# Kernel optimization log

Measured on AMD Instinct MI355X. Metric: run time of the kernel, lower is better.

Reference implementation:

```python
import jax, jax.numpy as jnp
import numpy as np

N_HEAD = 16
ROPE_BASE = 10000.0
RMS_EPS = 1e-6

def rms_norm(x):
    # F.rms_norm(x, (x.size(-1),)) -- no learned weight
    return x * jax.lax.rsqrt(jnp.mean(x * x, axis=-1, keepdims=True) + RMS_EPS)

def rope(x):
    # x: [B, T, H, hd]; rotate halves (non-interleaved) like the torch Rotary
    T, hd = x.shape[1], x.shape[3]
    d = hd // 2
    inv_freq = 1.0 / (ROPE_BASE ** (jnp.arange(0, hd, 2, dtype=jnp.float32) / hd))  # [d]
    t = jnp.arange(T, dtype=jnp.float32)
    freqs = jnp.outer(t, inv_freq)                       # [T, d]
    cos = jnp.cos(freqs)[None, :, None, :]
    sin = jnp.sin(freqs)[None, :, None, :]
    x1, x2 = x[..., :d], x[..., d:]
    y1 = x1 * cos + x2 * sin
    y2 = -x1 * sin + x2 * cos
    return jnp.concatenate([y1, y2], axis=-1).astype(x.dtype)

def setup_inputs() -> dict:
    key = jax.random.key(0)
    ks = jax.random.split(key, 7)
    B, T, D, H = 2, 2048, 1024, N_HEAD
    hd = D // H
    s = 0.02
    return {
        "x": jax.random.normal(ks[0], (B, T, D), jnp.float32),
        "v1": jax.random.normal(ks[1], (B, T, H, hd), jnp.float32),
        "w_q": jax.random.normal(ks[2], (D, D), jnp.float32) * s,
        "w_k": jax.random.normal(ks[3], (D, D), jnp.float32) * s,
        "w_v": jax.random.normal(ks[4], (D, D), jnp.float32) * s,
        "w_proj": jax.random.normal(ks[5], (D, D), jnp.float32) * s,
        "lamb": jnp.float32(0.5),
    }

def reference(x, v1, w_q, w_k, w_v, w_proj, lamb):
    B, T, D = x.shape
    H = N_HEAD
    hd = D // H
    q = (x @ w_q.T).reshape(B, T, H, hd)
    k = (x @ w_k.T).reshape(B, T, H, hd)
    v = (x @ w_v.T).reshape(B, T, H, hd)
    v = (1.0 - lamb) * v + lamb * v1.reshape(B, T, H, hd)
    q, k = rms_norm(q), rms_norm(k)
    q, k = rope(q), rope(k)
    scale = 1.0 / jnp.sqrt(jnp.float32(hd))
    scores = jnp.einsum('bqhd,bkhd->bhqk', q, k) * scale  # [B,H,T,T]
    causal = jnp.tril(jnp.ones((T, T), dtype=bool))
    scores = jnp.where(causal[None, None], scores, jnp.float32(-1e30))
    attn = jax.nn.softmax(scores, axis=-1)
    y = jnp.einsum('bhqk,bkhd->bqhd', attn, v).reshape(B, T, D)
    y = y @ w_proj.T
    return (y, v1)
```

## Files before the change

kernel.cpp:

```cpp
#include <hip/hip_runtime.h>

typedef __bf16 bf16x8 __attribute__((ext_vector_type(8)));
typedef float f32x4 __attribute__((ext_vector_type(4)));
typedef float f32x16 __attribute__((ext_vector_type(16)));

__device__ __forceinline__ unsigned short f2bf(float f) {
    return __builtin_bit_cast(unsigned short, (__bf16)f);
}

__device__ __forceinline__ float bf2f(unsigned short u) {
    unsigned int x = ((unsigned int)u) << 16;
    return __builtin_bit_cast(float, x);
}

__device__ __forceinline__ unsigned int packbf2(float a, float b) {
    unsigned short lo = f2bf(a), hi = f2bf(b);
    return (unsigned int)lo | ((unsigned int)hi << 16);
}

__device__ __forceinline__ bf16x8 load_frag(const unsigned short* p) {
    int4 v = *reinterpret_cast<const int4*>(p);
    return __builtin_bit_cast(bf16x8, v);
}

__device__ __forceinline__ void gload_lds16(const unsigned short* g, unsigned short* l) {
    __builtin_amdgcn_global_load_lds((const __attribute__((address_space(1))) void*)g,
                                     (__attribute__((address_space(3))) void*)l, 16, 0, 0);
}

__global__ __launch_bounds__(256) void prep_bf16(const float* __restrict__ x,
                                                 const float* __restrict__ wq,
                                                 const float* __restrict__ wk,
                                                 const float* __restrict__ wv,
                                                 const float* __restrict__ wp,
                                                 unsigned short* __restrict__ xb,
                                                 unsigned short* __restrict__ wall) {
    int i = (blockIdx.x * 256 + threadIdx.x) * 4;
    const float* src;
    unsigned short* dst;
    int soff, doff;
    if (i < (1 << 22)) {
        src = x; dst = xb; soff = i; doff = i;
    } else {
        int j = i - (1 << 22);
        int r = j >> 20;
        src = (r == 0) ? wq : ((r == 1) ? wk : ((r == 2) ? wv : wp));
        dst = wall; soff = j & 1048575; doff = j;
    }
    float4 v = *reinterpret_cast<const float4*>(&src[soff]);
    unsigned short tmp[4] = {f2bf(v.x), f2bf(v.y), f2bf(v.z), f2bf(v.w)};
    *reinterpret_cast<int2*>(&dst[doff]) = *reinterpret_cast<int2*>(tmp);
}

__global__ __launch_bounds__(256) void rope_table(float* __restrict__ cost,
                                                  float* __restrict__ sint) {
    int i = blockIdx.x * 256 + threadIdx.x;
    int t = i >> 5, d = i & 31;
    float inv = powf(10000.0f, -(float)d / 32.0f);
    float f = (float)t * inv;
    cost[i] = cosf(f);
    sint[i] = sinf(f);
}

template <bool BF16OUT>
__global__ __launch_bounds__(256) void gemm_bf16(const unsigned short* __restrict__ A,
                                                 const unsigned short* __restrict__ B,
                                                 void* __restrict__ Cv,
                                                 int N, int K) {
    __shared__ __align__(16) unsigned short As[128 * 64];
    __shared__ __align__(16) unsigned short Bs[128 * 64];
    int tid = threadIdx.x;
    int lane = tid & 63;
    int w = tid >> 6;
    int wm = w >> 1, wn = w & 1;
    int m0 = blockIdx.x * 128;
    int n0 = blockIdx.y * 128;

    f32x4 acc[4][4] = {};

    int r8 = lane >> 3;
    int csrc = (lane & 7) ^ r8;

    for (int k0 = 0; k0 < K; k0 += 64) {
        __syncthreads();
#pragma unroll
        for (int c = 0; c < 4; ++c) {
            int row = 32 * w + 8 * c + r8;
            gload_lds16(&A[(size_t)(m0 + row) * K + k0 + csrc * 8], &As[(32 * w + 8 * c) * 64]);
            gload_lds16(&B[(size_t)(n0 + row) * K + k0 + csrc * 8], &Bs[(32 * w + 8 * c) * 64]);
        }
        __syncthreads();
#pragma unroll
        for (int kk = 0; kk < 2; ++kk) {
            int col16 = kk * 4 + (lane >> 4);
            bf16x8 af[4], bfr[4];
#pragma unroll
            for (int i = 0; i < 4; ++i) {
                int row = wm * 64 + i * 16 + (lane & 15);
                af[i] = load_frag(&As[row * 64 + (col16 ^ (row & 7)) * 8]);
            }
#pragma unroll
            for (int j = 0; j < 4; ++j) {
                int row = wn * 64 + j * 16 + (lane & 15);
                bfr[j] = load_frag(&Bs[row * 64 + (col16 ^ (row & 7)) * 8]);
            }
#pragma unroll
            for (int i = 0; i < 4; ++i)
#pragma unroll
                for (int j = 0; j < 4; ++j)
                    acc[i][j] = __builtin_amdgcn_mfma_f32_16x16x32_bf16(af[i], bfr[j], acc[i][j], 0, 0, 0);
        }
    }
    int r0 = (lane >> 4) * 4;
    int cc = lane & 15;
#pragma unroll
    for (int i = 0; i < 4; ++i)
#pragma unroll
        for (int j = 0; j < 4; ++j)
#pragma unroll
            for (int r = 0; r < 4; ++r) {
                size_t m = m0 + wm * 64 + i * 16 + r0 + r;
                size_t n = n0 + wn * 64 + j * 16 + cc;
                if constexpr (BF16OUT) {
                    ((unsigned short*)Cv)[m * N + n] = f2bf(acc[i][j][r]);
                } else {
                    ((float*)Cv)[m * N + n] = acc[i][j][r];
                }
            }
}

__global__ __launch_bounds__(256) void postprocess_qk(const unsigned short* __restrict__ qkv,
                                                      const float* __restrict__ cost,
                                                      const float* __restrict__ sint,
                                                      unsigned short* __restrict__ qb,
                                                      unsigned short* __restrict__ kb) {
    int gid = blockIdx.x * 4 + (threadIdx.x >> 6);
    int lane = threadIdx.x & 63;
    int h = gid & 15;
    int t = (gid >> 4) & 2047;
    int b = gid >> 15;
    int m = b * 2048 + t;

    float q = bf2f(qkv[(size_t)m * 3072 + h * 64 + lane]);
    float k = bf2f(qkv[(size_t)m * 3072 + 1024 + h * 64 + lane]);

    float sq = q * q, sk = k * k;
    for (int msk = 1; msk < 64; msk <<= 1) {
        sq += __shfl_xor(sq, msk, 64);
        sk += __shfl_xor(sk, msk, 64);
    }
    q *= rsqrtf(sq * (1.0f / 64.0f) + 1e-6f);
    k *= rsqrtf(sk * (1.0f / 64.0f) + 1e-6f);

    int d = lane & 31;
    float c = cost[t * 32 + d], s = sint[t * 32 + d];
    float qp = __shfl_xor(q, 32, 64);
    float kp = __shfl_xor(k, 32, 64);
    float qo = (lane < 32) ? (q * c + qp * s) : (q * c - qp * s);
    float ko = (lane < 32) ? (k * c + kp * s) : (k * c - kp * s);
    qo *= 0.125f * 1.44269504088896f;

    size_t oidx = ((size_t)((b * 16 + h) * 2048 + t)) * 64 + lane;
    qb[oidx] = f2bf(qo);
    kb[oidx] = f2bf(ko);
}

__global__ __launch_bounds__(256) void lerp_transpose_v(const unsigned short* __restrict__ qkvb,
                                                        const float* __restrict__ v1,
                                                        const float* __restrict__ lamb_p,
                                                        unsigned short* __restrict__ vt,
                                                        float* __restrict__ outv1) {
    __shared__ __align__(16) unsigned short tile[64][72];
    int bh = blockIdx.y;
    int b = bh >> 4, h = bh & 15;
    int t0 = blockIdx.x * 64;
    int tid = threadIdx.x;
    int r = tid >> 3;
    int c = (tid & 7) * 8;
    float lamb = lamb_p[0];
    float oml = 1.0f - lamb;

#pragma unroll
    for (int half = 0; half < 2; ++half) {
        int row = r + half * 32;
        int m = b * 2048 + t0 + row;
        int4 vv = *reinterpret_cast<const int4*>(&qkvb[(size_t)m * 3072 + 2048 + h * 64 + c]);
        const unsigned short* vs = reinterpret_cast<const unsigned short*>(&vv);
        size_t v1i = ((size_t)m * 16 + h) * 64 + c;
        float4 va = *reinterpret_cast<const float4*>(&v1[v1i]);
        float4 vb4 = *reinterpret_cast<const float4*>(&v1[v1i + 4]);
        *reinterpret_cast<float4*>(&outv1[v1i]) = va;
        *reinterpret_cast<float4*>(&outv1[v1i + 4]) = vb4;
        float v1a[8] = {va.x, va.y, va.z, va.w, vb4.x, vb4.y, vb4.z, vb4.w};
        unsigned short tmp[8];
#pragma unroll
        for (int j = 0; j < 8; ++j) tmp[j] = f2bf(oml * bf2f(vs[j]) + lamb * v1a[j]);
        *reinterpret_cast<int4*>(&tile[row][c]) = *reinterpret_cast<int4*>(tmp);
    }
    __syncthreads();
    unsigned short* dst = vt + (size_t)bh * 64 * 2048 + t0;
    unsigned short tmp[8];
#pragma unroll
    for (int j = 0; j < 8; ++j) tmp[j] = tile[c + j][r];
    *reinterpret_cast<int4*>(&dst[(size_t)r * 2048 + c]) = *reinterpret_cast<int4*>(tmp);
#pragma unroll
    for (int j = 0; j < 8; ++j) tmp[j] = tile[c + j][r + 32];
    *reinterpret_cast<int4*>(&dst[(size_t)(r + 32) * 2048 + c]) = *reinterpret_cast<int4*>(tmp);
}

__global__ __launch_bounds__(256) void attn(const unsigned short* __restrict__ qb,
                                            const unsigned short* __restrict__ kb,
                                            const unsigned short* __restrict__ vt,
                                            unsigned short* __restrict__ pO,
                                            float* __restrict__ lsum) {
    __shared__ __align__(16) unsigned short Ks[64][72];
    __shared__ __align__(16) unsigned short Vt[64][72];
    int tid = threadIdx.x;
    int lane = tid & 63;
    int w = tid >> 6;
    int hi = lane >> 5;
    int l31 = lane & 31;

    int bid = blockIdx.x;
    int bh = bid & 31;
    int r5 = bid >> 5;
    int qt = 15 - (r5 >> 1);
    int ck = r5 & 1;
    int q0 = qt * 128;
    const size_t base = (size_t)bh * 2048 * 64;
    const unsigned short* vtb = vt + (size_t)bh * 64 * 2048;
    int ktlo = ck ? (qt + 1) : 0;
    int kthi = ck ? (2 * qt + 1) : qt;

    bf16x8 qf[4];
    int qrow = q0 + w * 32 + l31;
#pragma unroll
    for (int kd = 0; kd < 4; ++kd)
        qf[kd] = load_frag(&qb[base + (size_t)qrow * 64 + kd * 16 + hi * 8]);

    f32x16 oacc[2] = {};
    float lrun = 0.0f;

    int srow = tid >> 3;
    int scol = (tid & 7) * 8;
    int4 kr0, kr1, vr0, vr1;
#define LOADT(kt_)                                                                                    \
    do {                                                                                              \
        kr0 = *reinterpret_cast<const int4*>(&kb[base + (size_t)((kt_)*64 + srow) * 64 + scol]);      \
        kr1 = *reinterpret_cast<const int4*>(&kb[base + (size_t)((kt_)*64 + srow + 32) * 64 + scol]); \
        vr0 = *reinterpret_cast<const int4*>(&vtb[(size_t)srow * 2048 + (kt_)*64 + scol]);            \
        vr1 = *reinterpret_cast<const int4*>(&vtb[(size_t)(srow + 32) * 2048 + (kt_)*64 + scol]);     \
    } while (0)

    LOADT(ktlo);
    int qwlo = q0 + w * 32;

    for (int kt = ktlo; kt <= kthi; ++kt) {
        __syncthreads();
        *reinterpret_cast<int4*>(&Ks[srow][scol]) = kr0;
        *reinterpret_cast<int4*>(&Ks[srow + 32][scol]) = kr1;
        *reinterpret_cast<int4*>(&Vt[srow][scol]) = vr0;
        *reinterpret_cast<int4*>(&Vt[srow + 32][scol]) = vr1;
        __syncthreads();
        if (kt < kthi) LOADT(kt + 1);

        if (kt * 64 <= qwlo + 31) {
            f32x16 sacc[2] = {};
#pragma unroll
            for (int nt = 0; nt < 2; ++nt)
#pragma unroll
                for (int kd = 0; kd < 4; ++kd) {
                    bf16x8 kf = load_frag(&Ks[nt * 32 + l31][kd * 16 + hi * 8]);
                    sacc[nt] = __builtin_amdgcn_mfma_f32_32x32x16_bf16(kf, qf[kd], sacc[nt], 0, 0, 0);
                }

            bool diag = (kt * 64 + 63 > qwlo);
            float rs0 = 0.0f, rs1 = 0.0f, rs2 = 0.0f, rs3 = 0.0f;
#pragma unroll
            for (int nt = 0; nt < 2; ++nt)
#pragma unroll
                for (int r = 0; r < 16; ++r) {
                    float s = sacc[nt][r];
                    if (diag) {
                        int kvg = kt * 64 + nt * 32 + (r & 3) + 8 * (r >> 2) + 4 * hi;
                        if (kvg > qrow) s = -3.0e38f;
                    }
                    float e = __builtin_amdgcn_exp2f(s);
                    sacc[nt][r] = e;
                    if ((r & 3) == 0) rs0 += e;
                    else if ((r & 3) == 1) rs1 += e;
                    else if ((r & 3) == 2) rs2 += e;
                    else rs3 += e;
                }
            float rs = (rs0 + rs1) + (rs2 + rs3);
            rs += __shfl_xor(rs, 32, 64);
            lrun += rs;

            unsigned int wA[2][4], wB[2][4];
#pragma unroll
            for (int nt = 0; nt < 2; ++nt)
#pragma unroll
                for (int rr = 0; rr < 4; ++rr) {
                    wA[nt][rr] = packbf2(sacc[nt][4 * rr + 0], sacc[nt][4 * rr + 1]);
                    wB[nt][rr] = packbf2(sacc[nt][4 * rr + 2], sacc[nt][4 * rr + 3]);
                }

#pragma unroll
            for (int ks = 0; ks < 4; ++ks) {
                int nt = ks >> 1;
                int b2 = (ks & 1) * 2;
                auto rA = __builtin_amdgcn_permlane32_swap(wA[nt][b2], wA[nt][b2 + 1], false, false);
                auto rB = __builtin_amdgcn_permlane32_swap(wB[nt][b2], wB[nt][b2 + 1], false, false);
                uint4 pa;
                pa.x = rA[0];
                pa.y = rB[0];
                pa.z = rA[1];
                pa.w = rB[1];
                bf16x8 paf = __builtin_bit_cast(bf16x8, pa);
#pragma unroll
                for (int dt = 0; dt < 2; ++dt) {
                    bf16x8 vtf = load_frag(&Vt[dt * 32 + l31][ks * 16 + hi * 8]);
                    oacc[dt] = __builtin_amdgcn_mfma_f32_32x32x16_bf16(paf, vtf, oacc[dt], 0, 0, 0);
                }
            }
        }
    }

    unsigned short* po = pO + ((size_t)ck * 8388608u);
    float* ls = lsum + ck * 65536;
#pragma unroll
    for (int r = 0; r < 16; ++r) {
        int ql = (r & 3) + 8 * (r >> 2) + 4 * hi;
        int q = q0 + w * 32 + ql;
        size_t ro = ((size_t)bh * 2048 + q) * 64;
        po[ro + l31]      = f2bf(oacc[0][r]);
        po[ro + 32 + l31] = f2bf(oacc[1][r]);
    }
    if (hi == 0) ls[bh * 2048 + q0 + w * 32 + l31] = lrun;
#undef LOADT
}

__global__ __launch_bounds__(256) void combine(const unsigned short* __restrict__ pO,
                                               const float* __restrict__ lsum,
                                               unsigned short* __restrict__ yb) {
    int g = blockIdx.x * 256 + threadIdx.x;
    int d8 = (g & 7) * 8;
    int q  = (g >> 3) & 2047;
    int bh = g >> 14;
    int b = bh >> 4, h = bh & 15;
    size_t pi = ((size_t)bh * 2048 + q) * 64 + d8;
    int4 a = *reinterpret_cast<const int4*>(&pO[pi]);
    int4 c = *reinterpret_cast<const int4*>(&pO[8388608u + pi]);
    float l = lsum[bh * 2048 + q] + lsum[65536 + bh * 2048 + q];
    float linv = 1.0f / l;
    const unsigned short* ua = reinterpret_cast<const unsigned short*>(&a);
    const unsigned short* uc = reinterpret_cast<const unsigned short*>(&c);
    unsigned short tmp[8];
#pragma unroll
    for (int j = 0; j < 8; ++j) tmp[j] = f2bf((bf2f(ua[j]) + bf2f(uc[j])) * linv);
    *reinterpret_cast<int4*>(&yb[((size_t)(b * 2048 + q) * 16 + h) * 64 + d8]) =
        *reinterpret_cast<int4*>(tmp);
}

extern "C" void kernel_launch(void* const* d_in, const int* in_sizes, int n_in,
                              void* d_out, int out_size, void* d_ws, size_t ws_size,
                              hipStream_t stream) {
    const float* x      = (const float*)d_in[0];
    const float* v1     = (const float*)d_in[1];
    const float* w_q    = (const float*)d_in[2];
    const float* w_k    = (const float*)d_in[3];
    const float* w_v    = (const float*)d_in[4];
    const float* w_proj = (const float*)d_in[5];
    const float* lamb   = (const float*)d_in[6];
    float* out = (float*)d_out;

    char* ws = (char*)d_ws;
    unsigned short* xb      = (unsigned short*)(ws + 0);
    unsigned short* wall_b  = (unsigned short*)(ws + (8u  << 20));
    unsigned short* wqkv_b  = wall_b;
    unsigned short* wproj_b = wall_b + 3u * 1048576u;
    unsigned short* qkvb    = (unsigned short*)(ws + (16u << 20));
    unsigned short* vtp     = (unsigned short*)(ws + (40u << 20));
    unsigned short* qbuf    = (unsigned short*)(ws + (48u << 20));
    unsigned short* kbuf    = (unsigned short*)(ws + (56u << 20));
    unsigned short* ybuf    = (unsigned short*)(ws + (64u << 20));
    float*          cost    = (float*)        (ws + (72u << 20));
    float*          sint    = (float*)        (ws + (72u << 20) + 262144);
    unsigned short* pO      = (unsigned short*)(ws + 0);
    float*          lsum    = (float*)        (ws + (24u << 20));

    prep_bf16<<<8192, 256, 0, stream>>>(x, w_q, w_k, w_v, w_proj, xb, wall_b);
    rope_table<<<256, 256, 0, stream>>>(cost, sint);

    gemm_bf16<true><<<dim3(32, 24), 256, 0, stream>>>(xb, wqkv_b, (void*)qkvb, 3072, 1024);

    postprocess_qk<<<16384, 256, 0, stream>>>(qkvb, cost, sint, qbuf, kbuf);
    lerp_transpose_v<<<dim3(32, 32), 256, 0, stream>>>(qkvb, v1, lamb, vtp, out + 4194304);

    attn<<<1024, 256, 0, stream>>>(qbuf, kbuf, vtp, pO, lsum);
    combine<<<2048, 256, 0, stream>>>(pO, lsum, ybuf);

    gemm_bf16<false><<<dim3(32, 8), 256, 0, stream>>>(ybuf, wproj_b, (void*)out, 1024, 1024);
}
```

Before: 136.1 us.

## Split attention KV range into four chunks and merge small prep kernels

Attention now splits each query tile's causal key range into four balanced chunks instead of two, doubling the grid to 2048 blocks, and combine sums four partial outputs and row sums. The rope table kernel is folded into the bf16 conversion launch, and the q/k postprocess and v lerp/transpose kernels are merged into one launch. The aim is better occupancy and load balance in attention plus fewer launches. The cost is more partial-output traffic and a heavier combine step.

```diff
diff --git a/kernel.cpp b/kernel.cpp
--- a/kernel.cpp
+++ b/kernel.cpp
@@ -34,32 +34,34 @@
                                                  const float* __restrict__ wv,
                                                  const float* __restrict__ wp,
                                                  unsigned short* __restrict__ xb,
-                                                 unsigned short* __restrict__ wall) {
-    int i = (blockIdx.x * 256 + threadIdx.x) * 4;
-    const float* src;
-    unsigned short* dst;
-    int soff, doff;
-    if (i < (1 << 22)) {
-        src = x; dst = xb; soff = i; doff = i;
+                                                 unsigned short* __restrict__ wall,
+                                                 float* __restrict__ cost,
+                                                 float* __restrict__ sint) {
+    int bid = blockIdx.x;
+    if (bid < 8192) {
+        int i = (bid * 256 + threadIdx.x) * 4;
+        const float* src;
+        unsigned short* dst;
+        int soff, doff;
+        if (i < (1 << 22)) {
+            src = x; dst = xb; soff = i; doff = i;
+        } else {
+            int j = i - (1 << 22);
+            int r = j >> 20;
+            src = (r == 0) ? wq : ((r == 1) ? wk : ((r == 2) ? wv : wp));
+            dst = wall; soff = j & 1048575; doff = j;
+        }
+        float4 v = *reinterpret_cast<const float4*>(&src[soff]);
+        unsigned short tmp[4] = {f2bf(v.x), f2bf(v.y), f2bf(v.z), f2bf(v.w)};
+        *reinterpret_cast<int2*>(&dst[doff]) = *reinterpret_cast<int2*>(tmp);
     } else {
-        int j = i - (1 << 22);
-        int r = j >> 20;
-        src = (r == 0) ? wq : ((r == 1) ? wk : ((r == 2) ? wv : wp));
-        dst = wall; soff = j & 1048575; doff = j;
+        int i = (bid - 8192) * 256 + threadIdx.x;
+        int t = i >> 5, d = i & 31;
+        float inv = powf(10000.0f, -(float)d / 32.0f);
+        float f = (float)t * inv;
+        cost[i] = cosf(f);
+        sint[i] = sinf(f);
     }
-    float4 v = *reinterpret_cast<const float4*>(&src[soff]);
-    unsigned short tmp[4] = {f2bf(v.x), f2bf(v.y), f2bf(v.z), f2bf(v.w)};
-    *reinterpret_cast<int2*>(&dst[doff]) = *reinterpret_cast<int2*>(tmp);
-}
-
-__global__ __launch_bounds__(256) void rope_table(float* __restrict__ cost,
-                                                  float* __restrict__ sint) {
-    int i = blockIdx.x * 256 + threadIdx.x;
-    int t = i >> 5, d = i & 31;
-    float inv = powf(10000.0f, -(float)d / 32.0f);
-    float f = (float)t * inv;
-    cost[i] = cosf(f);
-    sint[i] = sinf(f);
 }
 
 template <bool BF16OUT>
@@ -129,83 +131,85 @@
             }
 }
 
-__global__ __launch_bounds__(256) void postprocess_qk(const unsigned short* __restrict__ qkv,
-                                                      const float* __restrict__ cost,
-                                                      const float* __restrict__ sint,
-                                                      unsigned short* __restrict__ qb,
-                                                      unsigned short* __restrict__ kb) {
-    int gid = blockIdx.x * 4 + (threadIdx.x >> 6);
-    int lane = threadIdx.x & 63;
-    int h = gid & 15;
-    int t = (gid >> 4) & 2047;
-    int b = gid >> 15;
-    int m = b * 2048 + t;
-
-    float q = bf2f(qkv[(size_t)m * 3072 + h * 64 + lane]);
-    float k = bf2f(qkv[(size_t)m * 3072 + 1024 + h * 64 + lane]);
-
-    float sq = q * q, sk = k * k;
-    for (int msk = 1; msk < 64; msk <<= 1) {
-        sq += __shfl_xor(sq, msk, 64);
-        sk += __shfl_xor(sk, msk, 64);
+__global__ __launch_bounds__(256) void post_lerp(const unsigned short* __restrict__ qkv,
+                                                 const float* __restrict__ cost,
+                                                 const float* __restrict__ sint,
+                                                 const float* __restrict__ v1,
+                                                 const float* __restrict__ lamb_p,
+                                                 unsigned short* __restrict__ qb,
+                                                 unsigned short* __restrict__ kb,
+                                                 unsigned short* __restrict__ vt,
+                                                 float* __restrict__ outv1) {
+    __shared__ __align__(16) unsigned short tile[64][72];
+    int bid = blockIdx.x;
+    if (bid < 16384) {
+        int gid = bid * 4 + (threadIdx.x >> 6);
+        int lane = threadIdx.x & 63;
+        int h = gid & 15;
+        int t = (gid >> 4) & 2047;
+        int b = gid >> 15;
+        int m = b * 2048 + t;
+
+        float q = bf2f(qkv[(size_t)m * 3072 + h * 64 + lane]);
+        float k = bf2f(qkv[(size_t)m * 3072 + 1024 + h * 64 + lane]);
+
+        float sq = q * q, sk = k * k;
+        for (int msk = 1; msk < 64; msk <<= 1) {
+            sq += __shfl_xor(sq, msk, 64);
+            sk += __shfl_xor(sk, msk, 64);
+        }
+        q *= rsqrtf(sq * (1.0f / 64.0f) + 1e-6f);
+        k *= rsqrtf(sk * (1.0f / 64.0f) + 1e-6f);
+
+        int d = lane & 31;
+        float c = cost[t * 32 + d], s = sint[t * 32 + d];
+        float qp = __shfl_xor(q, 32, 64);
+        float kp = __shfl_xor(k, 32, 64);
+        float qo = (lane < 32) ? (q * c + qp * s) : (q * c - qp * s);
+        float ko = (lane < 32) ? (k * c + kp * s) : (k * c - kp * s);
+        qo *= 0.125f * 1.44269504088896f;
+
+        size_t oidx = ((size_t)((b * 16 + h) * 2048 + t)) * 64 + lane;
+        qb[oidx] = f2bf(qo);
+        kb[oidx] = f2bf(ko);
+    } else {
+        int b2 = bid - 16384;
+        int bh = b2 >> 5;
+        int b = bh >> 4, h = bh & 15;
+        int t0 = (b2 & 31) * 64;
+        int tid = threadIdx.x;
+        int r = tid >> 3;
+        int c = (tid & 7) * 8;
+        float lamb = lamb_p[0];
+        float oml = 1.0f - lamb;
+
+#pragma unroll
+        for (int half = 0; half < 2; ++half) {
+            int row = r + half * 32;
+            int m = b * 2048 + t0 + row;
+            int4 vv = *reinterpret_cast<const int4*>(&qkv[(size_t)m * 3072 + 2048 + h * 64 + c]);
+            const unsigned short* vs = reinterpret_cast<const unsigned short*>(&vv);
+            size_t v1i = ((size_t)m * 16 + h) * 64 + c;
+            float4 va = *reinterpret_cast<const float4*>(&v1[v1i]);
+            float4 vb4 = *reinterpret_cast<const float4*>(&v1[v1i + 4]);
+            *reinterpret_cast<float4*>(&outv1[v1i]) = va;
+            *reinterpret_cast<float4*>(&outv1[v1i + 4]) = vb4;
+            float v1a[8] = {va.x, va.y, va.z, va.w, vb4.x, vb4.y, vb4.z, vb4.w};
+            unsigned short tmp[8];
+#pragma unroll
+            for (int j = 0; j < 8; ++j) tmp[j] = f2bf(oml * bf2f(vs[j]) + lamb * v1a[j]);
+            *reinterpret_cast<int4*>(&tile[row][c]) = *reinterpret_cast<int4*>(tmp);
+        }
+        __syncthreads();
+        unsigned short* dst = vt + (size_t)bh * 64 * 2048 + t0;
+        unsigned short tmp[8];
+#pragma unroll
+        for (int j = 0; j < 8; ++j) tmp[j] = tile[c + j][r];
+        *reinterpret_cast<int4*>(&dst[(size_t)r * 2048 + c]) = *reinterpret_cast<int4*>(tmp);
+#pragma unroll
+        for (int j = 0; j < 8; ++j) tmp[j] = tile[c + j][r + 32];
+        *reinterpret_cast<int4*>(&dst[(size_t)(r + 32) * 2048 + c]) = *reinterpret_cast<int4*>(tmp);
     }
-    q *= rsqrtf(sq * (1.0f / 64.0f) + 1e-6f);
-    k *= rsqrtf(sk * (1.0f / 64.0f) + 1e-6f);
-
-    int d = lane & 31;
-    float c = cost[t * 32 + d], s = sint[t * 32 + d];
-    float qp = __shfl_xor(q, 32, 64);
-    float kp = __shfl_xor(k, 32, 64);
-    float qo = (lane < 32) ? (q * c + qp * s) : (q * c - qp * s);
-    float ko = (lane < 32) ? (k * c + kp * s) : (k * c - kp * s);
-    qo *= 0.125f * 1.44269504088896f;
-
-    size_t oidx = ((size_t)((b * 16 + h) * 2048 + t)) * 64 + lane;
-    qb[oidx] = f2bf(qo);
-    kb[oidx] = f2bf(ko);
-}
-
-__global__ __launch_bounds__(256) void lerp_transpose_v(const unsigned short* __restrict__ qkvb,
-                                                        const float* __restrict__ v1,
-                                                        const float* __restrict__ lamb_p,
-                                                        unsigned short* __restrict__ vt,
-                                                        float* __restrict__ outv1) {
-    __shared__ __align__(16) unsigned short tile[64][72];
-    int bh = blockIdx.y;
-    int b = bh >> 4, h = bh & 15;
-    int t0 = blockIdx.x * 64;
-    int tid = threadIdx.x;
-    int r = tid >> 3;
-    int c = (tid & 7) * 8;
-    float lamb = lamb_p[0];
-    float oml = 1.0f - lamb;
-
-#pragma unroll
-    for (int half = 0; half < 2; ++half) {
-        int row = r + half * 32;
-        int m = b * 2048 + t0 + row;
-        int4 vv = *reinterpret_cast<const int4*>(&qkvb[(size_t)m * 3072 + 2048 + h * 64 + c]);
-        const unsigned short* vs = reinterpret_cast<const unsigned short*>(&vv);
-        size_t v1i = ((size_t)m * 16 + h) * 64 + c;
-        float4 va = *reinterpret_cast<const float4*>(&v1[v1i]);
-        float4 vb4 = *reinterpret_cast<const float4*>(&v1[v1i + 4]);
-        *reinterpret_cast<float4*>(&outv1[v1i]) = va;
-        *reinterpret_cast<float4*>(&outv1[v1i + 4]) = vb4;
-        float v1a[8] = {va.x, va.y, va.z, va.w, vb4.x, vb4.y, vb4.z, vb4.w};
-        unsigned short tmp[8];
-#pragma unroll
-        for (int j = 0; j < 8; ++j) tmp[j] = f2bf(oml * bf2f(vs[j]) + lamb * v1a[j]);
-        *reinterpret_cast<int4*>(&tile[row][c]) = *reinterpret_cast<int4*>(tmp);
-    }
-    __syncthreads();
-    unsigned short* dst = vt + (size_t)bh * 64 * 2048 + t0;
-    unsigned short tmp[8];
-#pragma unroll
-    for (int j = 0; j < 8; ++j) tmp[j] = tile[c + j][r];
-    *reinterpret_cast<int4*>(&dst[(size_t)r * 2048 + c]) = *reinterpret_cast<int4*>(tmp);
-#pragma unroll
-    for (int j = 0; j < 8; ++j) tmp[j] = tile[c + j][r + 32];
-    *reinterpret_cast<int4*>(&dst[(size_t)(r + 32) * 2048 + c]) = *reinterpret_cast<int4*>(tmp);
 }
 
 __global__ __launch_bounds__(256) void attn(const unsigned short* __restrict__ qb,
@@ -223,14 +227,15 @@
 
     int bid = blockIdx.x;
     int bh = bid & 31;
-    int r5 = bid >> 5;
-    int qt = 15 - (r5 >> 1);
-    int ck = r5 & 1;
+    int r6 = bid >> 5;
+    int qt = 15 - (r6 >> 2);
+    int ck = r6 & 3;
     int q0 = qt * 128;
     const size_t base = (size_t)bh * 2048 * 64;
     const unsigned short* vtb = vt + (size_t)bh * 64 * 2048;
-    int ktlo = ck ? (qt + 1) : 0;
-    int kthi = ck ? (2 * qt + 1) : qt;
+    int nt = 2 * qt + 2;
+    int ktlo = (ck * nt) >> 2;
+    int kthi = ((ck + 1) * nt) >> 2;
 
     bf16x8 qf[4];
     int qrow = q0 + w * 32 + l31;
@@ -252,81 +257,82 @@
         vr1 = *reinterpret_cast<const int4*>(&vtb[(size_t)(srow + 32) * 2048 + (kt_)*64 + scol]);     \
     } while (0)
 
-    LOADT(ktlo);
     int qwlo = q0 + w * 32;
-
-    for (int kt = ktlo; kt <= kthi; ++kt) {
-        __syncthreads();
-        *reinterpret_cast<int4*>(&Ks[srow][scol]) = kr0;
-        *reinterpret_cast<int4*>(&Ks[srow + 32][scol]) = kr1;
-        *reinterpret_cast<int4*>(&Vt[srow][scol]) = vr0;
-        *reinterpret_cast<int4*>(&Vt[srow + 32][scol]) = vr1;
-        __syncthreads();
-        if (kt < kthi) LOADT(kt + 1);
-
-        if (kt * 64 <= qwlo + 31) {
-            f32x16 sacc[2] = {};
-#pragma unroll
-            for (int nt = 0; nt < 2; ++nt)
-#pragma unroll
-                for (int kd = 0; kd < 4; ++kd) {
-                    bf16x8 kf = load_frag(&Ks[nt * 32 + l31][kd * 16 + hi * 8]);
-                    sacc[nt] = __builtin_amdgcn_mfma_f32_32x32x16_bf16(kf, qf[kd], sacc[nt], 0, 0, 0);
-                }
-
-            bool diag = (kt * 64 + 63 > qwlo);
-            float rs0 = 0.0f, rs1 = 0.0f, rs2 = 0.0f, rs3 = 0.0f;
-#pragma unroll
-            for (int nt = 0; nt < 2; ++nt)
-#pragma unroll
-                for (int r = 0; r < 16; ++r) {
-                    float s = sacc[nt][r];
-                    if (diag) {
-                        int kvg = kt * 64 + nt * 32 + (r & 3) + 8 * (r >> 2) + 4 * hi;
-                        if (kvg > qrow) s = -3.0e38f;
+    if (ktlo < kthi) {
+        LOADT(ktlo);
+        for (int kt = ktlo; kt < kthi; ++kt) {
+            __syncthreads();
+            *reinterpret_cast<int4*>(&Ks[srow][scol]) = kr0;
+            *reinterpret_cast<int4*>(&Ks[srow + 32][scol]) = kr1;
+            *reinterpret_cast<int4*>(&Vt[srow][scol]) = vr0;
+            *reinterpret_cast<int4*>(&Vt[srow + 32][scol]) = vr1;
+            __syncthreads();
+            if (kt + 1 < kthi) LOADT(kt + 1);
+
+            if (kt * 64 <= qwlo + 31) {
+                f32x16 sacc[2] = {};
+#pragma unroll
+                for (int ntl = 0; ntl < 2; ++ntl)
+#pragma unroll
+                    for (int kd = 0; kd < 4; ++kd) {
+                        bf16x8 kf = load_frag(&Ks[ntl * 32 + l31][kd * 16 + hi * 8]);
+                        sacc[ntl] = __builtin_amdgcn_mfma_f32_32x32x16_bf16(kf, qf[kd], sacc[ntl], 0, 0, 0);
                     }
-                    float e = __builtin_amdgcn_exp2f(s);
-                    sacc[nt][r] = e;
-                    if ((r & 3) == 0) rs0 += e;
-                    else if ((r & 3) == 1) rs1 += e;
-                    else if ((r & 3) == 2) rs2 += e;
-                    else rs3 += e;
-                }
-            float rs = (rs0 + rs1) + (rs2 + rs3);
-            rs += __shfl_xor(rs, 32, 64);
-            lrun += rs;
-
-            unsigned int wA[2][4], wB[2][4];
-#pragma unroll
-            for (int nt = 0; nt < 2; ++nt)
-#pragma unroll
-                for (int rr = 0; rr < 4; ++rr) {
-                    wA[nt][rr] = packbf2(sacc[nt][4 * rr + 0], sacc[nt][4 * rr + 1]);
-                    wB[nt][rr] = packbf2(sacc[nt][4 * rr + 2], sacc[nt][4 * rr + 3]);
-                }
-
-#pragma unroll
-            for (int ks = 0; ks < 4; ++ks) {
-                int nt = ks >> 1;
-                int b2 = (ks & 1) * 2;
-                auto rA = __builtin_amdgcn_permlane32_swap(wA[nt][b2], wA[nt][b2 + 1], false, false);
-                auto rB = __builtin_amdgcn_permlane32_swap(wB[nt][b2], wB[nt][b2 + 1], false, false);
-                uint4 pa;
-                pa.x = rA[0];
-                pa.y = rB[0];
-                pa.z = rA[1];
-                pa.w = rB[1];
-                bf16x8 paf = __builtin_bit_cast(bf16x8, pa);
-#pragma unroll
-                for (int dt = 0; dt < 2; ++dt) {
-                    bf16x8 vtf = load_frag(&Vt[dt * 32 + l31][ks * 16 + hi * 8]);
-                    oacc[dt] = __builtin_amdgcn_mfma_f32_32x32x16_bf16(paf, vtf, oacc[dt], 0, 0, 0);
+
+                bool diag = (kt * 64 + 63 > qwlo);
+                float rs0 = 0.0f, rs1 = 0.0f, rs2 = 0.0f, rs3 = 0.0f;
+#pragma unroll
+                for (int ntl = 0; ntl < 2; ++ntl)
+#pragma unroll
+                    for (int r = 0; r < 16; ++r) {
+                        float s = sacc[ntl][r];
+                        if (diag) {
+                            int kvg = kt * 64 + ntl * 32 + (r & 3) + 8 * (r >> 2) + 4 * hi;
+                            if (kvg > qrow) s = -3.0e38f;
+                        }
+                        float e = __builtin_amdgcn_exp2f(s);
+                        sacc[ntl][r] = e;
+                        if ((r & 3) == 0) rs0 += e;
+                        else if ((r & 3) == 1) rs1 += e;
+                        else if ((r & 3) == 2) rs2 += e;
+                        else rs3 += e;
+                    }
+                float rs = (rs0 + rs1) + (rs2 + rs3);
+                rs += __shfl_xor(rs, 32, 64);
+                lrun += rs;
+
+                unsigned int wA[2][4], wB[2][4];
+#pragma unroll
+                for (int ntl = 0; ntl < 2; ++ntl)
+#pragma unroll
+                    for (int rr = 0; rr < 4; ++rr) {
+                        wA[ntl][rr] = packbf2(sacc[ntl][4 * rr + 0], sacc[ntl][4 * rr + 1]);
+                        wB[ntl][rr] = packbf2(sacc[ntl][4 * rr + 2], sacc[ntl][4 * rr + 3]);
+                    }
+
+#pragma unroll
+                for (int ks = 0; ks < 4; ++ks) {
+                    int ntl = ks >> 1;
+                    int b2 = (ks & 1) * 2;
+                    auto rA = __builtin_amdgcn_permlane32_swap(wA[ntl][b2], wA[ntl][b2 + 1], false, false);
+                    auto rB = __builtin_amdgcn_permlane32_swap(wB[ntl][b2], wB[ntl][b2 + 1], false, false);
+                    uint4 pa;
+                    pa.x = rA[0];
+                    pa.y = rB[0];
+                    pa.z = rA[1];
+                    pa.w = rB[1];
+                    bf16x8 paf = __builtin_bit_cast(bf16x8, pa);
+#pragma unroll
+                    for (int dt = 0; dt < 2; ++dt) {
+                        bf16x8 vtf = load_frag(&Vt[dt * 32 + l31][ks * 16 + hi * 8]);
+                        oacc[dt] = __builtin_amdgcn_mfma_f32_32x32x16_bf16(paf, vtf, oacc[dt], 0, 0, 0);
+                    }
                 }
             }
         }
     }
 
-    unsigned short* po = pO + ((size_t)ck * 8388608u);
+    unsigned short* po = pO + ((size_t)ck * 4194304u);
     float* ls = lsum + ck * 65536;
 #pragma unroll
     for (int r = 0; r < 16; ++r) {
@@ -349,15 +355,21 @@
     int bh = g >> 14;
     int b = bh >> 4, h = bh & 15;
     size_t pi = ((size_t)bh * 2048 + q) * 64 + d8;
-    int4 a = *reinterpret_cast<const int4*>(&pO[pi]);
-    int4 c = *reinterpret_cast<const int4*>(&pO[8388608u + pi]);
-    float l = lsum[bh * 2048 + q] + lsum[65536 + bh * 2048 + q];
+    int4 p0 = *reinterpret_cast<const int4*>(&pO[pi]);
+    int4 p1 = *reinterpret_cast<const int4*>(&pO[4194304u + pi]);
+    int4 p2 = *reinterpret_cast<const int4*>(&pO[8388608u + pi]);
+    int4 p3 = *reinterpret_cast<const int4*>(&pO[12582912u + pi]);
+    int li = bh * 2048 + q;
+    float l = lsum[li] + lsum[65536 + li] + lsum[131072 + li] + lsum[196608 + li];
     float linv = 1.0f / l;
-    const unsigned short* ua = reinterpret_cast<const unsigned short*>(&a);
-    const unsigned short* uc = reinterpret_cast<const unsigned short*>(&c);
+    const unsigned short* u0 = reinterpret_cast<const unsigned short*>(&p0);
+    const unsigned short* u1 = reinterpret_cast<const unsigned short*>(&p1);
+    const unsigned short* u2 = reinterpret_cast<const unsigned short*>(&p2);
+    const unsigned short* u3 = reinterpret_cast<const unsigned short*>(&p3);
     unsigned short tmp[8];
 #pragma unroll
-    for (int j = 0; j < 8; ++j) tmp[j] = f2bf((bf2f(ua[j]) + bf2f(uc[j])) * linv);
+    for (int j = 0; j < 8; ++j)
+        tmp[j] = f2bf(((bf2f(u0[j]) + bf2f(u1[j])) + (bf2f(u2[j]) + bf2f(u3[j]))) * linv);
     *reinterpret_cast<int4*>(&yb[((size_t)(b * 2048 + q) * 16 + h) * 64 + d8]) =
         *reinterpret_cast<int4*>(tmp);
 }
@@ -386,18 +398,16 @@
     unsigned short* ybuf    = (unsigned short*)(ws + (64u << 20));
     float*          cost    = (float*)        (ws + (72u << 20));
     float*          sint    = (float*)        (ws + (72u << 20) + 262144);
-    unsigned short* pO      = (unsigned short*)(ws + 0);
-    float*          lsum    = (float*)        (ws + (24u << 20));
-
-    prep_bf16<<<8192, 256, 0, stream>>>(x, w_q, w_k, w_v, w_proj, xb, wall_b);
-    rope_table<<<256, 256, 0, stream>>>(cost, sint);
+    unsigned short* pO      = (unsigned short*)(ws + (80u << 20));
+    float*          lsum    = (float*)        (ws + (112u << 20));
+
+    prep_bf16<<<8448, 256, 0, stream>>>(x, w_q, w_k, w_v, w_proj, xb, wall_b, cost, sint);
 
     gemm_bf16<true><<<dim3(32, 24), 256, 0, stream>>>(xb, wqkv_b, (void*)qkvb, 3072, 1024);
 
-    postprocess_qk<<<16384, 256, 0, stream>>>(qkvb, cost, sint, qbuf, kbuf);
-    lerp_transpose_v<<<dim3(32, 32), 256, 0, stream>>>(qkvb, v1, lamb, vtp, out + 4194304);
-
-    attn<<<1024, 256, 0, stream>>>(qbuf, kbuf, vtp, pO, lsum);
+    post_lerp<<<17408, 256, 0, stream>>>(qkvb, cost, sint, v1, lamb, qbuf, kbuf, vtp, out + 4194304);
+
+    attn<<<2048, 256, 0, stream>>>(qbuf, kbuf, vtp, pO, lsum);
     combine<<<2048, 256, 0, stream>>>(pO, lsum, ybuf);
 
     gemm_bf16<false><<<dim3(32, 8), 256, 0, stream>>>(ybuf, wproj_b, (void*)out, 1024, 1024);
```

Result: no change. 134.4 us (-1.2%).
